# Optimization experiments

Measured on AMD Instinct MI355X. Metric: run time of the kernel, lower is better.

## Reference

```python
import jax, jax.numpy as jnp
import numpy as np

N = 50000; E = 800000; G = 256; F = 34; D = 128; H = 4; C = 32; L = 4
EPS = 1e-5

def _bn(x, g, b):
    # BatchNorm1d with batch statistics (train-mode math), eval dropout (identity)
    m = jnp.mean(x, 0); v = jnp.var(x, 0)
    return g * (x - m) * jax.lax.rsqrt(v + EPS) + b

def _seg_softmax(s, seg, n):
    # numerically-stable softmax over edges grouped by destination node
    m = jax.ops.segment_max(s, seg, num_segments=n)
    m = jnp.where(jnp.isfinite(m), m, 0.0)
    e = jnp.exp(s - m[seg])
    d = jax.ops.segment_sum(e, seg, num_segments=n)
    return e / (d[seg] + 1e-16)

def setup_inputs():
    key = jax.random.key(0)
    ks = iter(jax.random.split(key, 64))
    def rn(shape, s=0.05):
        return jax.random.normal(next(ks), shape, dtype=jnp.float32) * s
    inp = {}
    inp['x'] = jax.random.normal(next(ks), (N, F), dtype=jnp.float32)
    inp['edge_index'] = jax.random.randint(next(ks), (2, E), 0, N, dtype=jnp.int32)
    inp['batch'] = jnp.sort(jax.random.randint(next(ks), (N,), 0, G, dtype=jnp.int32))
    inp['emb_W'] = rn((F, D)); inp['emb_b'] = rn((D,))
    inp['emb_g'] = jnp.ones((D,)); inp['emb_be'] = jnp.zeros((D,))
    inp['gWl'] = rn((L, D, D)); inp['gWr'] = rn((L, D, D))
    inp['gbl'] = rn((L, D)); inp['gbr'] = rn((L, D))
    inp['gatt'] = rn((L, H, C)); inp['gbias'] = rn((L, D))
    inp['gg'] = jnp.ones((L, D)); inp['gbe'] = jnp.zeros((L, D))
    inp['tWq'] = rn((D, D)); inp['tWk'] = rn((D, D)); inp['tWv'] = rn((D, D)); inp['tWs'] = rn((D, D))
    inp['tbq'] = rn((D,)); inp['tbk'] = rn((D,)); inp['tbv'] = rn((D,)); inp['tbs'] = rn((D,))
    inp['tg'] = jnp.ones((D,)); inp['tbe'] = jnp.zeros((D,))
    inp['oW1'] = rn((2 * D, D)); inp['ob1'] = rn((D,))
    inp['og'] = jnp.ones((D,)); inp['obe'] = jnp.zeros((D,))
    inp['oW2'] = rn((D, D // 2)); inp['ob2'] = rn((D // 2,))
    inp['oW3'] = rn((D // 2, 1)); inp['ob3'] = rn((1,))
    return inp

def reference(x, edge_index, batch, emb_W, emb_b, emb_g, emb_be, gWl, gWr, gbl, gbr, gatt, gbias, gg, gbe, tWq, tWk, tWv, tWs, tbq, tbk, tbv, tbs, tg, tbe, oW1, ob1, og, obe, oW2, ob2, oW3, ob3):
    x = jax.nn.relu(_bn(x @ emb_W + emb_b, emb_g, emb_be))
    sl = jnp.arange(N, dtype=edge_index.dtype)
    ei = jnp.concatenate([edge_index, jnp.stack([sl, sl])], axis=1)  # GATv2 default add_self_loops=True
    src, dst = ei[0], ei[1]
    for l in range(L):  # 4 structurally identical GATv2 layers
        xl = (x @ gWl[l] + gbl[l]).reshape(N, H, C)
        xr = (x @ gWr[l] + gbr[l]).reshape(N, H, C)
        e = jax.nn.leaky_relu(xl[src] + xr[dst], 0.2)  # [E+N, H, C]
        sc = jnp.einsum('ehc,hc->eh', e, gatt[l])
        a = _seg_softmax(sc, dst, N)
        out = jax.ops.segment_sum(xl[src] * a[..., None], dst, num_segments=N).reshape(N, D) + gbias[l]
        x = x + jax.nn.relu(_bn(out, gg[l], gbe[l]))
    # TransformerConv: no self-loops by default, dot-product attention + root skip
    s2, d2 = edge_index[0], edge_index[1]
    q = (x @ tWq + tbq).reshape(N, H, C)
    k = (x @ tWk + tbk).reshape(N, H, C)
    v = (x @ tWv + tbv).reshape(N, H, C)
    sc = jnp.einsum('ehc,ehc->eh', q[d2], k[s2]) / np.float32(np.sqrt(C))
    a = _seg_softmax(sc, d2, N)
    agg = jax.ops.segment_sum(v[s2] * a[..., None], d2, num_segments=N).reshape(N, D)
    x = x + _bn(agg + x @ tWs + tbs, tg, tbe)
    # global mean + max pooling over graphs
    cnt = jax.ops.segment_sum(jnp.ones((N,), x.dtype), batch, num_segments=G)
    xm = jax.ops.segment_sum(x, batch, num_segments=G) / jnp.maximum(cnt, 1.0)[:, None]
    xx = jax.ops.segment_max(x, batch, num_segments=G)
    xx = jnp.where(jnp.isfinite(xx), xx, 0.0)  # guard empty segments
    h = jnp.concatenate([xm, xx], axis=1)
    h = jax.nn.relu(_bn(h @ oW1 + ob1, og, obe))
    h = jax.nn.relu(h @ oW2 + ob2)
    return h @ oW3 + ob3
```

## Files before the change

### kernel.cpp

```cpp
#include <hip/hip_runtime.h>
#include <hip/hip_fp16.h>

namespace {
constexpr int NN = 50000;
constexpr int NE = 800000;
constexpr int NG = 256;
constexpr int NF = 34;
constexpr int NL = 4;
constexpr int NB = (NN + 255) / 256;
constexpr int STS = 32;
constexpr int GQ = ((NE + 3) / 4 + 255) / 256;
constexpr int GE = (NN + 63) / 64;
}
#define EPSB 1e-5f
#define LSLOPE 0.2f
#define INV_SQRT_C 0.17677669529663687f

typedef short bf16x8 __attribute__((ext_vector_type(8)));
typedef float f32x4 __attribute__((ext_vector_type(4)));
typedef _Float16 hv2 __attribute__((ext_vector_type(2)));

static __device__ __forceinline__ short f2bf(float f) {
    unsigned int u = __float_as_uint(f);
    u = (u + 0x7fff + ((u >> 16) & 1)) >> 16;
    return (short)u;
}
static __device__ __forceinline__ unsigned fenc(float x) {
    unsigned u = __float_as_uint(x);
    return (u & 0x80000000u) ? ~u : (u | 0x80000000u);
}
static __device__ __forceinline__ float fdec(unsigned u) {
    return __uint_as_float((u & 0x80000000u) ? (u ^ 0x80000000u) : ~u);
}
static __device__ __forceinline__ float fdot2(hv2 a, hv2 b, float c) {
    return __builtin_amdgcn_fdot2(a, b, c, false);
}

__global__ __launch_bounds__(256) void k_init(const int* __restrict__ ei,
                                              int* __restrict__ deg,
                                              int* __restrict__ rank,
                                              const float* __restrict__ gWl,
                                              const float* __restrict__ gWr,
                                              const float* __restrict__ tWq,
                                              const float* __restrict__ tWk,
                                              const float* __restrict__ tWv,
                                              const float* __restrict__ tWs,
                                              short* __restrict__ Wt,
                                              const float* __restrict__ A,
                                              const float* __restrict__ W,
                                              const float* __restrict__ bias,
                                              float* __restrict__ outEmb,
                                              float* __restrict__ stms) {
    __shared__ float As[64 * NF];
    __shared__ float sred[256];
    int blk = blockIdx.x;
    if (blk < GQ) {
        int tid = blk * 256 + threadIdx.x;
        const int S = (NE + 3) / 4;
        if (tid >= S) return;
#pragma unroll
        for (int k = 0; k < 4; ++k) {
            int e = tid + k * S;
            if (e < NE) rank[e] = atomicAdd(&deg[ei[NE + e]], 1);
        }
        return;
    }
    blk -= GQ;
    if (blk < 12) {
        const float* src;
        if (blk < 4) src = gWl + blk * 16384;
        else if (blk < 8) src = gWr + (blk - 4) * 16384;
        else if (blk == 8) src = tWq;
        else if (blk == 9) src = tWk;
        else if (blk == 10) src = tWv;
        else src = tWs;
        short* d = Wt + blk * 16384;
        for (int i = threadIdx.x; i < 16384; i += 256) {
            int n = i >> 7, k = i & 127;
            d[i] = f2bf(src[k * 128 + n]);
        }
        return;
    }
    blk -= 12;
    int r0 = blk * 64;
    int rows = NN - r0; if (rows > 64) rows = 64;
    int total = rows * NF;
    for (int idx = threadIdx.x; idx < 64 * NF; idx += 256)
        As[idx] = (idx < total) ? A[(size_t)r0 * NF + idx] : 0.f;
    sred[threadIdx.x] = 0.f;
    __syncthreads();
    int tx = threadIdx.x & 31, ty = threadIdx.x >> 5;
    const float4* W4 = (const float4*)W;
    float acc[8][4];
#pragma unroll
    for (int j = 0; j < 8; ++j)
#pragma unroll
        for (int i = 0; i < 4; ++i) acc[j][i] = 0.f;
#pragma unroll 2
    for (int k = 0; k < NF; ++k) {
        float4 w = W4[k * 32 + tx];
#pragma unroll
        for (int j = 0; j < 8; ++j) {
            float a = As[(ty * 8 + j) * NF + k];
            acc[j][0] += a * w.x; acc[j][1] += a * w.y;
            acc[j][2] += a * w.z; acc[j][3] += a * w.w;
        }
    }
    float4 b = ((const float4*)bias)[tx];
    float s[4] = {0.f, 0.f, 0.f, 0.f}, ss[4] = {0.f, 0.f, 0.f, 0.f};
#pragma unroll
    for (int j = 0; j < 8; ++j) {
        int r = ty * 8 + j;
        if (r < rows) {
            float4 o = make_float4(acc[j][0] + b.x, acc[j][1] + b.y,
                                   acc[j][2] + b.z, acc[j][3] + b.w);
            ((float4*)outEmb)[(size_t)(r0 + r) * 32 + tx] = o;
            s[0] += o.x; ss[0] += o.x * o.x;
            s[1] += o.y; ss[1] += o.y * o.y;
            s[2] += o.z; ss[2] += o.z * o.z;
            s[3] += o.w; ss[3] += o.w * o.w;
        }
    }
#pragma unroll
    for (int i = 0; i < 4; ++i) {
        atomicAdd(&sred[tx * 4 + i], s[i]);
        atomicAdd(&sred[128 + tx * 4 + i], ss[i]);
    }
    __syncthreads();
    atomicAdd(&stms[(blk & (STS - 1)) * 256 + threadIdx.x], sred[threadIdx.x]);
}

__global__ __launch_bounds__(256) void k_scan1(const int* __restrict__ deg, int* __restrict__ bsum) {
    __shared__ int sm[256];
    int i = blockIdx.x * 256 + threadIdx.x;
    sm[threadIdx.x] = (i < NN) ? deg[i] : 0;
    __syncthreads();
    for (int off = 128; off > 0; off >>= 1) {
        if (threadIdx.x < off) sm[threadIdx.x] += sm[threadIdx.x + off];
        __syncthreads();
    }
    if (threadIdx.x == 0) bsum[blockIdx.x] = sm[0];
}

__global__ __launch_bounds__(256) void k_scan2(const int* __restrict__ bsum,
                                               int* __restrict__ boff, int* __restrict__ rp) {
    __shared__ int sm[256];
    int t = threadIdx.x;
    int v = (t < NB) ? bsum[t] : 0;
    sm[t] = v;
    __syncthreads();
    for (int off = 1; off < 256; off <<= 1) {
        int u = (t >= off) ? sm[t - off] : 0;
        __syncthreads();
        sm[t] += u;
        __syncthreads();
    }
    if (t < NB) boff[t] = sm[t] - v;
    if (t == 255) rp[NN] = sm[255];
}

__global__ __launch_bounds__(256) void k_scan3(const int* __restrict__ deg,
                                               const int* __restrict__ boff,
                                               int* __restrict__ rp) {
    __shared__ int sm[256];
    int i = blockIdx.x * 256 + threadIdx.x;
    int t = threadIdx.x;
    int v = (i < NN) ? deg[i] : 0;
    sm[t] = v;
    __syncthreads();
    for (int off = 1; off < 256; off <<= 1) {
        int u = (t >= off) ? sm[t - off] : 0;
        __syncthreads();
        sm[t] += u;
        __syncthreads();
    }
    if (i < NN) rp[i] = boff[blockIdx.x] + sm[t] - v;
}

__global__ __launch_bounds__(256) void k_fill(const int* __restrict__ ei,
                                              const int* __restrict__ rp,
                                              const int* __restrict__ rank,
                                              int* __restrict__ esrc) {
    int tid = blockIdx.x * 256 + threadIdx.x;
    const int S = (NE + 3) / 4;
    if (tid >= S) return;
#pragma unroll
    for (int k = 0; k < 4; ++k) {
        int e = tid + k * S;
        if (e < NE) {
            int s = ei[e];
            int d = ei[NE + e];
            int p = rp[d] + rank[e];
            esrc[p] = s;
        }
    }
}

__global__ __launch_bounds__(256) void k_stats(const __half* __restrict__ src, int nRows,
                                               float* __restrict__ st) {
    int c = threadIdx.x & 127;
    int sub = threadIdx.x >> 7;
    int r0 = blockIdx.x * 128;
    int rend = r0 + 128; if (rend > nRows) rend = nRows;
    float s = 0.f, ss = 0.f;
    for (int r = r0 + sub; r < rend; r += 2) {
        float v = __half2float(src[(size_t)r * 128 + c]);
        s += v; ss += v * v;
    }
    float* dst = st + (blockIdx.x & (STS - 1)) * 256;
    atomicAdd(&dst[c], s);
    atomicAdd(&dst[128 + c], ss);
}

template <int SRC16, int OUTH0, int OUTH1, int RES, int XOUT>
__global__ __launch_bounds__(256) void k_gemm2bn(const float* __restrict__ src,
                                                 const float* __restrict__ res,
                                                 float* __restrict__ xout,
                                                 const float* __restrict__ st,
                                                 const float* __restrict__ g,
                                                 const float* __restrict__ b,
                                                 const short* __restrict__ Wt0,
                                                 const short* __restrict__ Wt1,
                                                 const float* __restrict__ bias0,
                                                 const float* __restrict__ bias1,
                                                 void* __restrict__ out0,
                                                 void* __restrict__ out1, int nRows) {
    __shared__ short As[128 * 136];
    __shared__ short Bs[128 * 136];
    __shared__ float scsh[256];
    const float invn = 1.f / NN;
    if (threadIdx.x < 128) {
        int c = threadIdx.x;
        float s0v = 0.f, s1v = 0.f;
#pragma unroll 8
        for (int k2 = 0; k2 < STS; ++k2) {
            s0v += st[k2 * 256 + c];
            s1v += st[k2 * 256 + 128 + c];
        }
        float mean = s0v * invn;
        float var = fmaxf(s1v * invn - mean * mean, 0.f);
        float s = g[c] * rsqrtf(var + EPSB);
        scsh[c] = s;
        scsh[128 + c] = b[c] - mean * s;
    }
    {
        const int4* Wt4 = (const int4*)Wt0;
        for (int idx = threadIdx.x; idx < 2048; idx += 256) {
            int row = idx >> 4, c8 = idx & 15;
            *(int4*)&Bs[row * 136 + c8 * 8] = Wt4[idx];
        }
    }
    __syncthreads();
    int r0 = blockIdx.x * 128;
    int rows = nRows - r0; if (rows > 128) rows = 128;
    for (int idx = threadIdx.x; idx < 2048; idx += 256) {
        int r = idx >> 4, c8 = idx & 15;
        short4 sa = {0, 0, 0, 0}, sb = {0, 0, 0, 0};
        if (r < rows) {
            size_t base = (size_t)(r0 + r) * 128 + c8 * 8;
            float4 v0, v1;
            if (SRC16) {
                union { float4 f4; __half h[8]; } u;
                u.f4 = *(const float4*)&((const __half*)src)[base];
                v0 = make_float4(__half2float(u.h[0]), __half2float(u.h[1]),
                                 __half2float(u.h[2]), __half2float(u.h[3]));
                v1 = make_float4(__half2float(u.h[4]), __half2float(u.h[5]),
                                 __half2float(u.h[6]), __half2float(u.h[7]));
            } else {
                v0 = *(const float4*)&src[base];
                v1 = *(const float4*)&src[base + 4];
            }
            int c = c8 * 8;
            v0.x = fmaxf(v0.x * scsh[c + 0] + scsh[128 + c + 0], 0.f);
            v0.y = fmaxf(v0.y * scsh[c + 1] + scsh[128 + c + 1], 0.f);
            v0.z = fmaxf(v0.z * scsh[c + 2] + scsh[128 + c + 2], 0.f);
            v0.w = fmaxf(v0.w * scsh[c + 3] + scsh[128 + c + 3], 0.f);
            v1.x = fmaxf(v1.x * scsh[c + 4] + scsh[128 + c + 4], 0.f);
            v1.y = fmaxf(v1.y * scsh[c + 5] + scsh[128 + c + 5], 0.f);
            v1.z = fmaxf(v1.z * scsh[c + 6] + scsh[128 + c + 6], 0.f);
            v1.w = fmaxf(v1.w * scsh[c + 7] + scsh[128 + c + 7], 0.f);
            if (RES) {
                float4 rr0 = *(const float4*)&res[base];
                float4 rr1 = *(const float4*)&res[base + 4];
                v0.x += rr0.x; v0.y += rr0.y; v0.z += rr0.z; v0.w += rr0.w;
                v1.x += rr1.x; v1.y += rr1.y; v1.z += rr1.z; v1.w += rr1.w;
            }
            if (XOUT) {
                *(float4*)&xout[base] = v0;
                *(float4*)&xout[base + 4] = v1;
            }
            sa.x = f2bf(v0.x); sa.y = f2bf(v0.y); sa.z = f2bf(v0.z); sa.w = f2bf(v0.w);
            sb.x = f2bf(v1.x); sb.y = f2bf(v1.y); sb.z = f2bf(v1.z); sb.w = f2bf(v1.w);
        }
        *(short4*)&As[r * 136 + c8 * 8] = sa;
        *(short4*)&As[r * 136 + c8 * 8 + 4] = sb;
    }
    __syncthreads();
    int lane = threadIdx.x & 63, wave = threadIdx.x >> 6;
    int n16 = lane & 15, quad = lane >> 4;
    bf16x8 af[2][4];
#pragma unroll
    for (int rt = 0; rt < 2; ++rt)
#pragma unroll
        for (int kc = 0; kc < 4; ++kc)
            af[rt][kc] = *(const bf16x8*)&As[(wave * 32 + rt * 16 + n16) * 136 + kc * 32 + quad * 8];

    f32x4 acc[2][8];
#pragma unroll
    for (int rt = 0; rt < 2; ++rt)
#pragma unroll
        for (int ct = 0; ct < 8; ++ct) acc[rt][ct] = (f32x4){0.f, 0.f, 0.f, 0.f};
#pragma unroll
    for (int ct = 0; ct < 8; ++ct)
#pragma unroll
        for (int kc = 0; kc < 4; ++kc) {
            bf16x8 bf = *(const bf16x8*)&Bs[(ct * 16 + n16) * 136 + kc * 32 + quad * 8];
            acc[0][ct] = __builtin_amdgcn_mfma_f32_16x16x32_bf16(af[0][kc], bf, acc[0][ct], 0, 0, 0);
            acc[1][ct] = __builtin_amdgcn_mfma_f32_16x16x32_bf16(af[1][kc], bf, acc[1][ct], 0, 0, 0);
        }
#pragma unroll
    for (int ct = 0; ct < 8; ++ct) {
        int colI = ct * 16 + n16;
        float bv = bias0[colI];
#pragma unroll
        for (int rt = 0; rt < 2; ++rt)
#pragma unroll
            for (int reg = 0; reg < 4; ++reg) {
                int r = wave * 32 + rt * 16 + quad * 4 + reg;
                if (r < rows) {
                    float v = acc[rt][ct][reg] + bv;
                    if (OUTH0) ((__half*)out0)[(size_t)(r0 + r) * 128 + colI] = __float2half(v);
                    else       ((float*)out0)[(size_t)(r0 + r) * 128 + colI] = v;
                }
            }
    }
    __syncthreads();
    {
        const int4* Wt4 = (const int4*)Wt1;
        for (int idx = threadIdx.x; idx < 2048; idx += 256) {
            int row = idx >> 4, c8 = idx & 15;
            *(int4*)&Bs[row * 136 + c8 * 8] = Wt4[idx];
        }
    }
    __syncthreads();
#pragma unroll
    for (int rt = 0; rt < 2; ++rt)
#pragma unroll
        for (int ct = 0; ct < 8; ++ct) acc[rt][ct] = (f32x4){0.f, 0.f, 0.f, 0.f};
#pragma unroll
    for (int ct = 0; ct < 8; ++ct)
#pragma unroll
        for (int kc = 0; kc < 4; ++kc) {
            bf16x8 bf = *(const bf16x8*)&Bs[(ct * 16 + n16) * 136 + kc * 32 + quad * 8];
            acc[0][ct] = __builtin_amdgcn_mfma_f32_16x16x32_bf16(af[0][kc], bf, acc[0][ct], 0, 0, 0);
            acc[1][ct] = __builtin_amdgcn_mfma_f32_16x16x32_bf16(af[1][kc], bf, acc[1][ct], 0, 0, 0);
        }
#pragma unroll
    for (int ct = 0; ct < 8; ++ct) {
        int colI = ct * 16 + n16;
        float bv = bias1[colI];
#pragma unroll
        for (int rt = 0; rt < 2; ++rt)
#pragma unroll
            for (int reg = 0; reg < 4; ++reg) {
                int r = wave * 32 + rt * 16 + quad * 4 + reg;
                if (r < rows) {
                    float v = acc[rt][ct][reg] + bv;
                    if (OUTH1) ((__half*)out1)[(size_t)(r0 + r) * 128 + colI] = __float2half(v);
                    else       ((float*)out1)[(size_t)(r0 + r) * 128 + colI] = v;
                }
            }
    }
}

__global__ __launch_bounds__(256) void k_gemm4bn(const __half* __restrict__ src,
                                                 const float* __restrict__ res,
                                                 float* __restrict__ xout,
                                                 const float* __restrict__ st,
                                                 const float* __restrict__ g,
                                                 const float* __restrict__ b,
                                                 const short* __restrict__ Wt,
                                                 const float* __restrict__ bq,
                                                 const float* __restrict__ bk,
                                                 const float* __restrict__ bv,
                                                 const float* __restrict__ bs,
                                                 __half* __restrict__ oq,
                                                 __half* __restrict__ ok,
                                                 __half* __restrict__ ov,
                                                 __half* __restrict__ os, int nRows) {
    __shared__ short As[128 * 136];
    __shared__ short Bs[128 * 136];
    __shared__ float scsh[256];
    const float invn = 1.f / NN;
    if (threadIdx.x < 128) {
        int c = threadIdx.x;
        float s0v = 0.f, s1v = 0.f;
#pragma unroll 8
        for (int k2 = 0; k2 < STS; ++k2) {
            s0v += st[k2 * 256 + c];
            s1v += st[k2 * 256 + 128 + c];
        }
        float mean = s0v * invn;
        float var = fmaxf(s1v * invn - mean * mean, 0.f);
        float s = g[c] * rsqrtf(var + EPSB);
        scsh[c] = s;
        scsh[128 + c] = b[c] - mean * s;
    }
    __syncthreads();
    int r0 = blockIdx.x * 128;
    int rows = nRows - r0; if (rows > 128) rows = 128;
    for (int idx = threadIdx.x; idx < 2048; idx += 256) {
        int r = idx >> 4, c8 = idx & 15;
        short4 sa = {0, 0, 0, 0}, sb = {0, 0, 0, 0};
        if (r < rows) {
            size_t base = (size_t)(r0 + r) * 128 + c8 * 8;
            union { float4 f4; __half h[8]; } u;
            u.f4 = *(const float4*)&src[base];
            float4 v0 = make_float4(__half2float(u.h[0]), __half2float(u.h[1]),
                                    __half2float(u.h[2]), __half2float(u.h[3]));
            float4 v1 = make_float4(__half2float(u.h[4]), __half2float(u.h[5]),
                                    __half2float(u.h[6]), __half2float(u.h[7]));
            int c = c8 * 8;
            v0.x = fmaxf(v0.x * scsh[c + 0] + scsh[128 + c + 0], 0.f);
            v0.y = fmaxf(v0.y * scsh[c + 1] + scsh[128 + c + 1], 0.f);
            v0.z = fmaxf(v0.z * scsh[c + 2] + scsh[128 + c + 2], 0.f);
            v0.w = fmaxf(v0.w * scsh[c + 3] + scsh[128 + c + 3], 0.f);
            v1.x = fmaxf(v1.x * scsh[c + 4] + scsh[128 + c + 4], 0.f);
            v1.y = fmaxf(v1.y * scsh[c + 5] + scsh[128 + c + 5], 0.f);
            v1.z = fmaxf(v1.z * scsh[c + 6] + scsh[128 + c + 6], 0.f);
            v1.w = fmaxf(v1.w * scsh[c + 7] + scsh[128 + c + 7], 0.f);
            float4 rr0 = *(const float4*)&res[base];
            float4 rr1 = *(const float4*)&res[base + 4];
            v0.x += rr0.x; v0.y += rr0.y; v0.z += rr0.z; v0.w += rr0.w;
            v1.x += rr1.x; v1.y += rr1.y; v1.z += rr1.z; v1.w += rr1.w;
            *(float4*)&xout[base] = v0;
            *(float4*)&xout[base + 4] = v1;
            sa.x = f2bf(v0.x); sa.y = f2bf(v0.y); sa.z = f2bf(v0.z); sa.w = f2bf(v0.w);
            sb.x = f2bf(v1.x); sb.y = f2bf(v1.y); sb.z = f2bf(v1.z); sb.w = f2bf(v1.w);
        }
        *(short4*)&As[r * 136 + c8 * 8] = sa;
        *(short4*)&As[r * 136 + c8 * 8 + 4] = sb;
    }
    int lane = threadIdx.x & 63, wave = threadIdx.x >> 6;
    int n16 = lane & 15, quad = lane >> 4;
    __half* outs[4] = {oq, ok, ov, os};
    const float* biases[4] = {bq, bk, bv, bs};
    bf16x8 af[2][4];
    bool afLoaded = false;
    for (int m = 0; m < 4; ++m) {
        {
            const int4* Wt4 = (const int4*)(Wt + (size_t)m * 16384);
            for (int idx = threadIdx.x; idx < 2048; idx += 256) {
                int row = idx >> 4, c8 = idx & 15;
                *(int4*)&Bs[row * 136 + c8 * 8] = Wt4[idx];
            }
        }
        __syncthreads();
        if (!afLoaded) {
            afLoaded = true;
#pragma unroll
            for (int rt = 0; rt < 2; ++rt)
#pragma unroll
                for (int kc = 0; kc < 4; ++kc)
                    af[rt][kc] = *(const bf16x8*)&As[(wave * 32 + rt * 16 + n16) * 136 + kc * 32 + quad * 8];
        }
        f32x4 acc[2][8];
#pragma unroll
        for (int rt = 0; rt < 2; ++rt)
#pragma unroll
            for (int ct = 0; ct < 8; ++ct) acc[rt][ct] = (f32x4){0.f, 0.f, 0.f, 0.f};
#pragma unroll
        for (int ct = 0; ct < 8; ++ct)
#pragma unroll
            for (int kc = 0; kc < 4; ++kc) {
                bf16x8 bf = *(const bf16x8*)&Bs[(ct * 16 + n16) * 136 + kc * 32 + quad * 8];
                acc[0][ct] = __builtin_amdgcn_mfma_f32_16x16x32_bf16(af[0][kc], bf, acc[0][ct], 0, 0, 0);
                acc[1][ct] = __builtin_amdgcn_mfma_f32_16x16x32_bf16(af[1][kc], bf, acc[1][ct], 0, 0, 0);
            }
        __half* om = outs[m];
        const float* bm = biases[m];
#pragma unroll
        for (int ct = 0; ct < 8; ++ct) {
            int colI = ct * 16 + n16;
            float bv2 = bm[colI];
#pragma unroll
            for (int rt = 0; rt < 2; ++rt)
#pragma unroll
                for (int reg = 0; reg < 4; ++reg) {
                    int r = wave * 32 + rt * 16 + quad * 4 + reg;
                    if (r < rows)
                        om[(size_t)(r0 + r) * 128 + colI] = __float2half(acc[rt][ct][reg] + bv2);
                }
        }
        if (m < 3) __syncthreads();
    }
}

__global__ __launch_bounds__(256) void k_gat_aggr(const __half* __restrict__ xl,
                                                  const __half* __restrict__ xr,
                                                  const float* __restrict__ att,
                                                  const float* __restrict__ gbias_l,
                                                  const int* __restrict__ rp,
                                                  const int* __restrict__ esrc,
                                                  __half* __restrict__ out) {
    int lane = threadIdx.x & 63;
    int node = blockIdx.x * 4 + (threadIdx.x >> 6);
    if (node >= NN) return;
    int q = lane >> 4;
    int l16 = lane & 15;
    int c8 = l16 * 8;
    float4 xrr = *(const float4*)&xr[(unsigned)node * 128u + c8];
    hv2 xrh[4] = {*(hv2*)&xrr.x, *(hv2*)&xrr.y, *(hv2*)&xrr.z, *(hv2*)&xrr.w};
    float4 atA = *(const float4*)&att[c8];
    float4 atB = *(const float4*)&att[c8 + 4];
    hv2 ath[4] = {{(_Float16)atA.x, (_Float16)atA.y}, {(_Float16)atA.z, (_Float16)atA.w},
                  {(_Float16)atB.x, (_Float16)atB.y}, {(_Float16)atB.z, (_Float16)atB.w}};
    const hv2 hz = {(_Float16)0.f, (_Float16)0.f};
    const hv2 hs = {(_Float16)LSLOPE, (_Float16)LSLOPE};
    int s0 = rp[node];
    int T = rp[node + 1] - s0 + 1;
    float a[8] = {0.f, 0.f, 0.f, 0.f, 0.f, 0.f, 0.f, 0.f};
    float l = 0.f;
    auto body = [&](int j) {
        bool self = (j == T - 1);
        int srcn = self ? node : esrc[s0 + j];
        float4 raw = *(const float4*)&xl[(unsigned)srcn * 128u + c8];
        hv2 f[4] = {*(hv2*)&raw.x, *(hv2*)&raw.y, *(hv2*)&raw.z, *(hv2*)&raw.w};
        float p = 0.f;
#pragma unroll
        for (int k = 0; k < 4; ++k) {
            hv2 e = f[k] + xrh[k];
            hv2 lk = __builtin_elementwise_max(e, hz) + hs * __builtin_elementwise_min(e, hz);
            p = fdot2(lk, ath[k], p);
        }
        p += __shfl_xor(p, 1); p += __shfl_xor(p, 2);
        float w = __expf(p);
#pragma unroll
        for (int k = 0; k < 4; ++k) {
            a[2 * k] += w * (float)f[k].x;
            a[2 * k + 1] += w * (float)f[k].y;
        }
        l += w;
    };
    int j = q;
    for (; j + 12 < T; j += 16) { body(j); body(j + 4); body(j + 8); body(j + 12); }
    for (; j + 4 < T; j += 8) { body(j); body(j + 4); }
    for (; j < T; j += 4) body(j);
#pragma unroll
    for (int k = 0; k < 8; ++k) { a[k] += __shfl_xor(a[k], 16); a[k] += __shfl_xor(a[k], 32); }
    l += __shfl_xor(l, 16); l += __shfl_xor(l, 32);
    if (q == 0) {
        float inv = 1.f / (l + 1e-16f);
        float4 gb0 = *(const float4*)&gbias_l[c8];
        float4 gb1 = *(const float4*)&gbias_l[c8 + 4];
        union { float4 f4; __half h[8]; } u;
        u.h[0] = __float2half(a[0] * inv + gb0.x); u.h[1] = __float2half(a[1] * inv + gb0.y);
        u.h[2] = __float2half(a[2] * inv + gb0.z); u.h[3] = __float2half(a[3] * inv + gb0.w);
        u.h[4] = __float2half(a[4] * inv + gb1.x); u.h[5] = __float2half(a[5] * inv + gb1.y);
        u.h[6] = __float2half(a[6] * inv + gb1.z); u.h[7] = __float2half(a[7] * inv + gb1.w);
        *(float4*)&out[(unsigned)node * 128u + c8] = u.f4;
    }
}

__global__ __launch_bounds__(256) void k_trans_aggr(const __half* __restrict__ qh,
                                                    const __half* __restrict__ kh,
                                                    const __half* __restrict__ vv,
                                                    const __half* __restrict__ sT,
                                                    const int* __restrict__ rp,
                                                    const int* __restrict__ esrc,
                                                    __half* __restrict__ out) {
    int lane = threadIdx.x & 63;
    int node = blockIdx.x * 4 + (threadIdx.x >> 6);
    if (node >= NN) return;
    int q = lane >> 4;
    int l16 = lane & 15;
    int c8 = l16 * 8;
    float4 qr = *(const float4*)&qh[(unsigned)node * 128u + c8];
    const hv2 hinv = {(_Float16)INV_SQRT_C, (_Float16)INV_SQRT_C};
    hv2 qv[4] = {(*(hv2*)&qr.x) * hinv, (*(hv2*)&qr.y) * hinv,
                 (*(hv2*)&qr.z) * hinv, (*(hv2*)&qr.w) * hinv};
    int s0 = rp[node];
    int T = rp[node + 1] - s0;
    float a[8] = {0.f, 0.f, 0.f, 0.f, 0.f, 0.f, 0.f, 0.f};
    float l = 0.f;
    auto body = [&](int j) {
        int srcn = esrc[s0 + j];
        float4 kraw = *(const float4*)&kh[(unsigned)srcn * 128u + c8];
        float4 vraw = *(const float4*)&vv[(unsigned)srcn * 128u + c8];
        hv2 kv[4] = {*(hv2*)&kraw.x, *(hv2*)&kraw.y, *(hv2*)&kraw.z, *(hv2*)&kraw.w};
        float p = 0.f;
#pragma unroll
        for (int k = 0; k < 4; ++k) p = fdot2(kv[k], qv[k], p);
        p += __shfl_xor(p, 1); p += __shfl_xor(p, 2);
        float w = __expf(p);
        hv2 vvv[4] = {*(hv2*)&vraw.x, *(hv2*)&vraw.y, *(hv2*)&vraw.z, *(hv2*)&vraw.w};
#pragma unroll
        for (int k = 0; k < 4; ++k) {
            a[2 * k] += w * (float)vvv[k].x;
            a[2 * k + 1] += w * (float)vvv[k].y;
        }
        l += w;
    };
    int j = q;
    for (; j + 12 < T; j += 16) { body(j); body(j + 4); body(j + 8); body(j + 12); }
    for (; j + 4 < T; j += 8) { body(j); body(j + 4); }
    for (; j < T; j += 4) body(j);
#pragma unroll
    for (int k = 0; k < 8; ++k) { a[k] += __shfl_xor(a[k], 16); a[k] += __shfl_xor(a[k], 32); }
    l += __shfl_xor(l, 16); l += __shfl_xor(l, 32);
    if (q == 0) {
        float inv = 1.f / (l + 1e-16f);
        float4 straw = *(const float4*)&sT[(unsigned)node * 128u + c8];
        hv2 st[4] = {*(hv2*)&straw.x, *(hv2*)&straw.y, *(hv2*)&straw.z, *(hv2*)&straw.w};
        union { float4 f4; __half h[8]; } u;
        u.h[0] = __float2half(a[0] * inv + (float)st[0].x);
        u.h[1] = __float2half(a[1] * inv + (float)st[0].y);
        u.h[2] = __float2half(a[2] * inv + (float)st[1].x);
        u.h[3] = __float2half(a[3] * inv + (float)st[1].y);
        u.h[4] = __float2half(a[4] * inv + (float)st[2].x);
        u.h[5] = __float2half(a[5] * inv + (float)st[2].y);
        u.h[6] = __float2half(a[6] * inv + (float)st[3].x);
        u.h[7] = __float2half(a[7] * inv + (float)st[3].y);
        *(float4*)&out[(unsigned)node * 128u + c8] = u.f4;
    }
}

__global__ __launch_bounds__(256) void k_pool_part(const __half* __restrict__ src,
                                                   const float* __restrict__ res,
                                                   const float* __restrict__ st,
                                                   const float* __restrict__ g,
                                                   const float* __restrict__ b,
                                                   const int* __restrict__ batch,
                                                   float* __restrict__ psum,
                                                   unsigned* __restrict__ pmax) {
    __shared__ int bs[64];
    __shared__ float sc_sh[128], sh_sh[128];
    int r0 = blockIdx.x * 64;
    if (threadIdx.x < 64) {
        int r = r0 + threadIdx.x;
        bs[threadIdx.x] = (r < NN) ? batch[r] : -1;
    }
    const float invn = 1.f / NN;
    if (threadIdx.x < 128) {
        int c2 = threadIdx.x;
        float s0v = 0.f, s1v = 0.f;
#pragma unroll 8
        for (int k2 = 0; k2 < STS; ++k2) {
            s0v += st[k2 * 256 + c2];
            s1v += st[k2 * 256 + 128 + c2];
        }
        float mean = s0v * invn;
        float var = fmaxf(s1v * invn - mean * mean, 0.f);
        float scv = g[c2] * rsqrtf(var + EPSB);
        sc_sh[c2] = scv;
        sh_sh[c2] = b[c2] - mean * scv;
    }
    __syncthreads();
    int c = threadIdx.x & 127;
    int sub = threadIdx.x >> 7;
    float scv = sc_sh[c];
    float shv = sh_sh[c];
    int curg = -1;
    float s = 0.f, fmx = -INFINITY;
    for (int i = sub; i < 64; i += 2) {
        int r = r0 + i;
        if (r >= NN) break;
        int gr = bs[i];
        if (gr != curg) {
            if (curg >= 0) {
                atomicAdd(&psum[curg * 128 + c], s);
                atomicMax(&pmax[curg * 128 + c], fenc(fmx));
            }
            curg = gr; s = 0.f; fmx = -INFINITY;
        }
        float v = __half2float(src[(size_t)r * 128 + c]) * scv + shv + res[(size_t)r * 128 + c];
        s += v; fmx = fmaxf(fmx, v);
    }
    if (curg >= 0) {
        atomicAdd(&psum[curg * 128 + c], s);
        atomicMax(&pmax[curg * 128 + c], fenc(fmx));
    }
}

__global__ __launch_bounds__(128) void k_pool_head1(const float* __restrict__ psum,
                                                    const unsigned* __restrict__ pmax,
                                                    const int* __restrict__ batch,
                                                    const float* __restrict__ W,
                                                    const float* __restrict__ b,
                                                    float* __restrict__ t1,
                                                    float* __restrict__ st6) {
    __shared__ float hr[256];
    __shared__ int se[2];
    int g = blockIdx.x;
    int t = threadIdx.x;
    if (t == 0) {
        int lo = 0, hi = NN;
        while (lo < hi) { int mid = (lo + hi) >> 1; if (batch[mid] < g) lo = mid + 1; else hi = mid; }
        se[0] = lo;
        hi = NN;
        while (lo < hi) { int mid = (lo + hi) >> 1; if (batch[mid] < g + 1) lo = mid + 1; else hi = mid; }
        se[1] = lo;
    }
    __syncthreads();
    int cnt = se[1] - se[0];
    float xm = psum[g * 128 + t] / fmaxf((float)cnt, 1.f);
    float xx = (cnt > 0) ? fdec(pmax[g * 128 + t]) : 0.f;
    hr[t] = xm;
    hr[128 + t] = xx;
    __syncthreads();
    float acc = b[t];
#pragma unroll 4
    for (int k = 0; k < 256; ++k) acc += hr[k] * W[k * 128 + t];
    t1[g * 128 + t] = acc;
    atomicAdd(&st6[t], acc);
    atomicAdd(&st6[128 + t], acc * acc);
}

__global__ __launch_bounds__(64) void k_head2(const float* __restrict__ t1,
                                              const float* __restrict__ st,
                                              const float* __restrict__ og,
                                              const float* __restrict__ obe,
                                              const float* __restrict__ W2,
                                              const float* __restrict__ b2,
                                              const float* __restrict__ W3,
                                              const float* __restrict__ b3,
                                              float* __restrict__ out) {
    __shared__ float v[128];
    int row = blockIdx.x, t = threadIdx.x;
    const float invn = 1.f / NG;
#pragma unroll
    for (int half = 0; half < 2; ++half) {
        int ch = t + half * 64;
        float mean = st[ch] * invn;
        float var = fmaxf(st[128 + ch] * invn - mean * mean, 0.f);
        float scv = og[ch] * rsqrtf(var + EPSB);
        float shv = obe[ch] - mean * scv;
        float a = t1[row * 128 + ch] * scv + shv;
        v[ch] = fmaxf(a, 0.f);
    }
    __syncthreads();
    float acc = b2[t];
#pragma unroll 4
    for (int k = 0; k < 128; ++k) acc += v[k] * W2[k * 64 + t];
    float p = fmaxf(acc, 0.f) * W3[t];
    p += __shfl_xor(p, 1); p += __shfl_xor(p, 2); p += __shfl_xor(p, 4);
    p += __shfl_xor(p, 8); p += __shfl_xor(p, 16); p += __shfl_xor(p, 32);
    if (t == 0) out[row] = p + b3[0];
}

extern "C" void kernel_launch(void* const* d_in, const int* in_sizes, int n_in,
                              void* d_out, int out_size, void* d_ws, size_t ws_size,
                              hipStream_t stream) {
    const float* x_in   = (const float*)d_in[0];
    const int*   ei     = (const int*)d_in[1];
    const int*   batch  = (const int*)d_in[2];
    const float* emb_W  = (const float*)d_in[3];
    const float* emb_b  = (const float*)d_in[4];
    const float* emb_g  = (const float*)d_in[5];
    const float* emb_be = (const float*)d_in[6];
    const float* gWl    = (const float*)d_in[7];
    const float* gWr    = (const float*)d_in[8];
    const float* gbl    = (const float*)d_in[9];
    const float* gbr    = (const float*)d_in[10];
    const float* gatt   = (const float*)d_in[11];
    const float* gbias  = (const float*)d_in[12];
    const float* gg     = (const float*)d_in[13];
    const float* gbe    = (const float*)d_in[14];
    const float* tWq    = (const float*)d_in[15];
    const float* tWk    = (const float*)d_in[16];
    const float* tWv    = (const float*)d_in[17];
    const float* tWs    = (const float*)d_in[18];
    const float* tbq    = (const float*)d_in[19];
    const float* tbk    = (const float*)d_in[20];
    const float* tbv    = (const float*)d_in[21];
    const float* tbs    = (const float*)d_in[22];
    const float* tg     = (const float*)d_in[23];
    const float* tbe    = (const float*)d_in[24];
    const float* oW1    = (const float*)d_in[25];
    const float* ob1    = (const float*)d_in[26];
    const float* og     = (const float*)d_in[27];
    const float* obe    = (const float*)d_in[28];
    const float* oW2    = (const float*)d_in[29];
    const float* ob2    = (const float*)d_in[30];
    const float* oW3    = (const float*)d_in[31];
    const float* ob3    = (const float*)d_in[32];
    float* out = (float*)d_out;

    const size_t NDsz = (size_t)NN * 128;
    float* x     = (float*)d_ws;
    float* bA    = x + NDsz;
    float* bC    = bA + NDsz;
    float* stats = bC + NDsz;
    float* hpool = stats + 7 * 256;
    float* t1    = hpool + 65536;
    float* scb   = t1 + 32768;
    __half* xlh  = (__half*)(scb + (size_t)(NE + NN) * 4);
    __half* xrh  = xlh + NDsz;
    __half* vh   = xrh + NDsz;
    __half* sh   = vh + NDsz;
    short* Wt    = (short*)(sh + NDsz);
    int* deg     = (int*)(Wt + 12 * 16384);
    int* rp      = deg + NN;
    int* cursor  = rp + NN + 1;
    int2* edg    = (int2*)(cursor + NN);
    int* bsum    = (int*)(edg + NE + 64);
    int* boff    = bsum + 256;
    float* psum  = (float*)(boff + 256);
    unsigned* pmax = (unsigned*)(psum + NG * 128);
    int* rank    = (int*)scb;
    int* esrc    = (int*)edg;
    float* stms  = scb + NE;
    __half* bCh  = (__half*)bC;

    hipMemsetAsync(deg, 0, NN * sizeof(int), stream);
    hipMemsetAsync(stats + 6 * 256, 0, 256 * sizeof(float), stream);
    hipMemsetAsync(stms, 0, 6 * STS * 256 * sizeof(float), stream);
    hipMemsetAsync(psum, 0, NG * 128 * 2 * sizeof(float), stream);

    const int gGemm = (NN + 127) / 128;
    const int gStat = (NN + 127) / 128;
    const int gNode = (NN + 3) / 4;
    const int gPool = (NN + 63) / 64;
    const int REG = STS * 256;

    k_init<<<GQ + 12 + GE, 256, 0, stream>>>(ei, deg, rank, gWl, gWr, tWq, tWk, tWv, tWs,
                                             Wt, x_in, emb_W, emb_b, bA, stms + 0 * REG);

    k_scan1<<<NB, 256, 0, stream>>>(deg, bsum);
    k_scan2<<<1, 256, 0, stream>>>(bsum, boff, rp);
    k_scan3<<<NB, 256, 0, stream>>>(deg, boff, rp);
    k_fill<<<GQ, 256, 0, stream>>>(ei, rp, rank, esrc);

    k_gemm2bn<0, 1, 1, 0, 1><<<gGemm, 256, 0, stream>>>(bA, nullptr, x, stms + 0 * REG, emb_g, emb_be,
                                                        Wt + (size_t)0 * 16384, Wt + (size_t)4 * 16384,
                                                        gbl + 0 * 128, gbr + 0 * 128, xlh, xrh, NN);
    k_gat_aggr<<<gNode, 256, 0, stream>>>(xlh, xrh, gatt + 0 * 128, gbias + 0 * 128, rp, esrc, bCh);
    k_stats<<<gStat, 256, 0, stream>>>(bCh, NN, stms + 1 * REG);
    k_gemm2bn<1, 1, 1, 1, 1><<<gGemm, 256, 0, stream>>>((const float*)bCh, x, bA, stms + 1 * REG, gg + 0 * 128, gbe + 0 * 128,
                                                        Wt + (size_t)1 * 16384, Wt + (size_t)5 * 16384,
                                                        gbl + 1 * 128, gbr + 1 * 128, xlh, xrh, NN);
    k_gat_aggr<<<gNode, 256, 0, stream>>>(xlh, xrh, gatt + 1 * 128, gbias + 1 * 128, rp, esrc, bCh);
    k_stats<<<gStat, 256, 0, stream>>>(bCh, NN, stms + 2 * REG);
    k_gemm2bn<1, 1, 1, 1, 1><<<gGemm, 256, 0, stream>>>((const float*)bCh, bA, x, stms + 2 * REG, gg + 1 * 128, gbe + 1 * 128,
                                                        Wt + (size_t)2 * 16384, Wt + (size_t)6 * 16384,
                                                        gbl + 2 * 128, gbr + 2 * 128, xlh, xrh, NN);
    k_gat_aggr<<<gNode, 256, 0, stream>>>(xlh, xrh, gatt + 2 * 128, gbias + 2 * 128, rp, esrc, bCh);
    k_stats<<<gStat, 256, 0, stream>>>(bCh, NN, stms + 3 * REG);
    k_gemm2bn<1, 1, 1, 1, 1><<<gGemm, 256, 0, stream>>>((const float*)bCh, x, bA, stms + 3 * REG, gg + 2 * 128, gbe + 2 * 128,
                                                        Wt + (size_t)3 * 16384, Wt + (size_t)7 * 16384,
                                                        gbl + 3 * 128, gbr + 3 * 128, xlh, xrh, NN);
    k_gat_aggr<<<gNode, 256, 0, stream>>>(xlh, xrh, gatt + 3 * 128, gbias + 3 * 128, rp, esrc, bCh);
    k_stats<<<gStat, 256, 0, stream>>>(bCh, NN, stms + 4 * REG);

    k_gemm4bn<<<gGemm, 256, 0, stream>>>(bCh, bA, x, stms + 4 * REG, gg + 3 * 128, gbe + 3 * 128,
                                         Wt + (size_t)8 * 16384, tbq, tbk, tbv, tbs,
                                         xrh, xlh, vh, sh, NN);
    k_trans_aggr<<<gNode, 256, 0, stream>>>(xrh, xlh, vh, sh, rp, esrc, bCh);
    k_stats<<<gStat, 256, 0, stream>>>(bCh, NN, stms + 5 * REG);

    k_pool_part<<<gPool, 256, 0, stream>>>(bCh, x, stms + 5 * REG, tg, tbe, batch, psum, pmax);
    k_pool_head1<<<NG, 128, 0, stream>>>(psum, pmax, batch, oW1, ob1, t1, stats + 6 * 256);
    k_head2<<<NG, 64, 0, stream>>>(t1, stats + 6 * 256, og, obe, oW2, ob2, oW3, ob3, out);
}
```

Before: 784.5 us.

## Split degree kernel, store embedding in fp16, interleave K/V for transformer aggregation

Moves the degree/rank atomic counting out of k_init into its own kernel with 8 edges per thread. The embedding output is stored as fp16 into the half buffer, and the first gemm reads it through the half-input path, which halves traffic for that tensor. K and V are written interleaved per node (stride 256) so the transformer aggregation gathers both from one contiguous row per source. The fp16 embedding adds rounding before batch norm, and vh must be large enough to hold the interleaved K/V.

```diff
diff --git a/kernel.cpp b/kernel.cpp
--- a/kernel.cpp
+++ b/kernel.cpp
@@ -10,6 +10,7 @@
 constexpr int NB = (NN + 255) / 256;
 constexpr int STS = 32;
 constexpr int GQ = ((NE + 3) / 4 + 255) / 256;
+constexpr int GD = ((NE + 7) / 8 + 255) / 256;
 constexpr int GE = (NN + 63) / 64;
 }
 #define EPSB 1e-5f
@@ -36,10 +37,20 @@
     return __builtin_amdgcn_fdot2(a, b, c, false);
 }
 
-__global__ __launch_bounds__(256) void k_init(const int* __restrict__ ei,
-                                              int* __restrict__ deg,
-                                              int* __restrict__ rank,
-                                              const float* __restrict__ gWl,
+__global__ __launch_bounds__(256) void k_deg(const int* __restrict__ ei,
+                                             int* __restrict__ deg,
+                                             int* __restrict__ rank) {
+    int tid = blockIdx.x * 256 + threadIdx.x;
+    const int S = (NE + 7) / 8;
+    if (tid >= S) return;
+#pragma unroll
+    for (int k = 0; k < 8; ++k) {
+        int e = tid + k * S;
+        if (e < NE) rank[e] = atomicAdd(&deg[ei[NE + e]], 1);
+    }
+}
+
+__global__ __launch_bounds__(256) void k_init(const float* __restrict__ gWl,
                                               const float* __restrict__ gWr,
                                               const float* __restrict__ tWq,
                                               const float* __restrict__ tWk,
@@ -49,23 +60,11 @@
                                               const float* __restrict__ A,
                                               const float* __restrict__ W,
                                               const float* __restrict__ bias,
-                                              float* __restrict__ outEmb,
+                                              __half* __restrict__ outEmb,
                                               float* __restrict__ stms) {
     __shared__ float As[64 * NF];
     __shared__ float sred[256];
     int blk = blockIdx.x;
-    if (blk < GQ) {
-        int tid = blk * 256 + threadIdx.x;
-        const int S = (NE + 3) / 4;
-        if (tid >= S) return;
-#pragma unroll
-        for (int k = 0; k < 4; ++k) {
-            int e = tid + k * S;
-            if (e < NE) rank[e] = atomicAdd(&deg[ei[NE + e]], 1);
-        }
-        return;
-    }
-    blk -= GQ;
     if (blk < 12) {
         const float* src;
         if (blk < 4) src = gWl + blk * 16384;
@@ -114,7 +113,10 @@
         if (r < rows) {
             float4 o = make_float4(acc[j][0] + b.x, acc[j][1] + b.y,
                                    acc[j][2] + b.z, acc[j][3] + b.w);
-            ((float4*)outEmb)[(size_t)(r0 + r) * 32 + tx] = o;
+            union { short4 s4; __half h[4]; } uh;
+            uh.h[0] = __float2half(o.x); uh.h[1] = __float2half(o.y);
+            uh.h[2] = __float2half(o.z); uh.h[3] = __float2half(o.w);
+            *(short4*)&outEmb[(size_t)(r0 + r) * 128 + tx * 4] = uh.s4;
             s[0] += o.x; ss[0] += o.x * o.x;
             s[1] += o.y; ss[1] += o.y * o.y;
             s[2] += o.z; ss[2] += o.z * o.z;
@@ -385,8 +387,7 @@
                                                  const float* __restrict__ bv,
                                                  const float* __restrict__ bs,
                                                  __half* __restrict__ oq,
-                                                 __half* __restrict__ ok,
-                                                 __half* __restrict__ ov,
+                                                 __half* __restrict__ okv,
                                                  __half* __restrict__ os, int nRows) {
     __shared__ short As[128 * 136];
     __shared__ short Bs[128 * 136];
@@ -443,8 +444,6 @@
     }
     int lane = threadIdx.x & 63, wave = threadIdx.x >> 6;
     int n16 = lane & 15, quad = lane >> 4;
-    __half* outs[4] = {oq, ok, ov, os};
-    const float* biases[4] = {bq, bk, bv, bs};
     bf16x8 af[2][4];
     bool afLoaded = false;
     for (int m = 0; m < 4; ++m) {
@@ -477,8 +476,12 @@
                 acc[0][ct] = __builtin_amdgcn_mfma_f32_16x16x32_bf16(af[0][kc], bf, acc[0][ct], 0, 0, 0);
                 acc[1][ct] = __builtin_amdgcn_mfma_f32_16x16x32_bf16(af[1][kc], bf, acc[1][ct], 0, 0, 0);
             }
-        __half* om = outs[m];
-        const float* bm = biases[m];
+        __half* om; int strd, off;
+        const float* bm;
+        if (m == 0)      { om = oq;  strd = 128; off = 0;   bm = bq; }
+        else if (m == 1) { om = okv; strd = 256; off = 0;   bm = bk; }
+        else if (m == 2) { om = okv; strd = 256; off = 128; bm = bv; }
+        else             { om = os;  strd = 128; off = 0;   bm = bs; }
 #pragma unroll
         for (int ct = 0; ct < 8; ++ct) {
             int colI = ct * 16 + n16;
@@ -489,7 +492,7 @@
                 for (int reg = 0; reg < 4; ++reg) {
                     int r = wave * 32 + rt * 16 + quad * 4 + reg;
                     if (r < rows)
-                        om[(size_t)(r0 + r) * 128 + colI] = __float2half(acc[rt][ct][reg] + bv2);
+                        om[(size_t)(r0 + r) * strd + off + colI] = __float2half(acc[rt][ct][reg] + bv2);
                 }
         }
         if (m < 3) __syncthreads();
@@ -563,8 +566,7 @@
 }
 
 __global__ __launch_bounds__(256) void k_trans_aggr(const __half* __restrict__ qh,
-                                                    const __half* __restrict__ kh,
-                                                    const __half* __restrict__ vv,
+                                                    const __half* __restrict__ kv,
                                                     const __half* __restrict__ sT,
                                                     const int* __restrict__ rp,
                                                     const int* __restrict__ esrc,
@@ -585,12 +587,13 @@
     float l = 0.f;
     auto body = [&](int j) {
         int srcn = esrc[s0 + j];
-        float4 kraw = *(const float4*)&kh[(unsigned)srcn * 128u + c8];
-        float4 vraw = *(const float4*)&vv[(unsigned)srcn * 128u + c8];
-        hv2 kv[4] = {*(hv2*)&kraw.x, *(hv2*)&kraw.y, *(hv2*)&kraw.z, *(hv2*)&kraw.w};
+        const __half* kvp = &kv[(unsigned)srcn * 256u + c8];
+        float4 kraw = *(const float4*)kvp;
+        float4 vraw = *(const float4*)(kvp + 128);
+        hv2 kvv[4] = {*(hv2*)&kraw.x, *(hv2*)&kraw.y, *(hv2*)&kraw.z, *(hv2*)&kraw.w};
         float p = 0.f;
 #pragma unroll
-        for (int k = 0; k < 4; ++k) p = fdot2(kv[k], qv[k], p);
+        for (int k = 0; k < 4; ++k) p = fdot2(kvv[k], qv[k], p);
         p += __shfl_xor(p, 1); p += __shfl_xor(p, 2);
         float w = __expf(p);
         hv2 vvv[4] = {*(hv2*)&vraw.x, *(hv2*)&vraw.y, *(hv2*)&vraw.z, *(hv2*)&vraw.w};
@@ -811,6 +814,7 @@
     int* esrc    = (int*)edg;
     float* stms  = scb + NE;
     __half* bCh  = (__half*)bC;
+    __half* kvh  = vh;
 
     hipMemsetAsync(deg, 0, NN * sizeof(int), stream);
     hipMemsetAsync(stats + 6 * 256, 0, 256 * sizeof(float), stream);
@@ -823,15 +827,16 @@
     const int gPool = (NN + 63) / 64;
     const int REG = STS * 256;
 
-    k_init<<<GQ + 12 + GE, 256, 0, stream>>>(ei, deg, rank, gWl, gWr, tWq, tWk, tWv, tWs,
-                                             Wt, x_in, emb_W, emb_b, bA, stms + 0 * REG);
+    k_deg<<<GD, 256, 0, stream>>>(ei, deg, rank);
+    k_init<<<12 + GE, 256, 0, stream>>>(gWl, gWr, tWq, tWk, tWv, tWs,
+                                        Wt, x_in, emb_W, emb_b, bCh, stms + 0 * REG);
 
     k_scan1<<<NB, 256, 0, stream>>>(deg, bsum);
     k_scan2<<<1, 256, 0, stream>>>(bsum, boff, rp);
     k_scan3<<<NB, 256, 0, stream>>>(deg, boff, rp);
     k_fill<<<GQ, 256, 0, stream>>>(ei, rp, rank, esrc);
 
-    k_gemm2bn<0, 1, 1, 0, 1><<<gGemm, 256, 0, stream>>>(bA, nullptr, x, stms + 0 * REG, emb_g, emb_be,
+    k_gemm2bn<1, 1, 1, 0, 1><<<gGemm, 256, 0, stream>>>((const float*)bCh, nullptr, x, stms + 0 * REG, emb_g, emb_be,
                                                         Wt + (size_t)0 * 16384, Wt + (size_t)4 * 16384,
                                                         gbl + 0 * 128, gbr + 0 * 128, xlh, xrh, NN);
     k_gat_aggr<<<gNode, 256, 0, stream>>>(xlh, xrh, gatt + 0 * 128, gbias + 0 * 128, rp, esrc, bCh);
@@ -854,8 +859,8 @@
 
     k_gemm4bn<<<gGemm, 256, 0, stream>>>(bCh, bA, x, stms + 4 * REG, gg + 3 * 128, gbe + 3 * 128,
                                          Wt + (size_t)8 * 16384, tbq, tbk, tbv, tbs,
-                                         xrh, xlh, vh, sh, NN);
-    k_trans_aggr<<<gNode, 256, 0, stream>>>(xrh, xlh, vh, sh, rp, esrc, bCh);
+                                         xrh, kvh, xlh, NN);
+    k_trans_aggr<<<gNode, 256, 0, stream>>>(xrh, kvh, xlh, rp, esrc, bCh);
     k_stats<<<gStat, 256, 0, stream>>>(bCh, NN, stms + 5 * REG);
 
     k_pool_part<<<gPool, 256, 0, stream>>>(bCh, x, stms + 5 * REG, tg, tbe, batch, psum, pmax);
```

After: 792.7 us. No clear change (+1.0%).
